# Optimization experiments

Hardware: AMD Instinct MI355X
Metric: run time of the kernel (lower is better)

Reference implementation:

```python
import jax, jax.numpy as jnp
import numpy as np

B, T, C = 2, 2048, 1024
NH = 16

def setup_inputs() -> dict:
    key = jax.random.key(0)
    ks = jax.random.split(key, 5)
    s = 0.02
    return {
        "x": jax.random.normal(ks[0], (B, T, C), dtype=jnp.float32),
        "w_attn": jax.random.normal(ks[1], (C, 3 * C), dtype=jnp.float32) * s,
        "b_attn": jax.random.normal(ks[2], (3 * C,), dtype=jnp.float32) * s,
        "w_proj": jax.random.normal(ks[3], (C, C), dtype=jnp.float32) * s,
        "b_proj": jax.random.normal(ks[4], (C,), dtype=jnp.float32) * s,
        "n_heads": NH,
    }

def reference(x, w_attn, b_attn, w_proj, b_proj, n_heads):
    Bx, Tx, Cx = x.shape
    hd = Cx // n_heads
    qkv = x @ w_attn + b_attn                      # [B,T,3C]
    q, k, v = jnp.split(qkv, 3, axis=-1)
    # [B,T,H,hd] -> [B,H,T,hd]
    q = q.reshape(Bx, Tx, n_heads, hd).transpose(0, 2, 1, 3)
    k = k.reshape(Bx, Tx, n_heads, hd).transpose(0, 2, 1, 3)
    v = v.reshape(Bx, Tx, n_heads, hd).transpose(0, 2, 1, 3)
    scale = 1.0 / np.sqrt(hd).astype(np.float32)
    att = jnp.einsum('bhqd,bhkd->bhqk', q, k) * scale   # [B,H,T,T]
    causal = jnp.tril(jnp.ones((Tx, Tx), dtype=bool))
    att = jnp.where(causal[None, None], att, -jnp.inf)
    att = jax.nn.softmax(att, axis=-1)
    y = jnp.einsum('bhqk,bhkd->bhqd', att, v)            # [B,H,T,hd]
    y = y.transpose(0, 2, 1, 3).reshape(Bx, Tx, Cx)
    return y @ w_proj + b_proj
```

## Files before the change

kernel.cpp:

```cpp
#include <hip/hip_runtime.h>

typedef __bf16 bf16x8 __attribute__((ext_vector_type(8)));
typedef __bf16 bf16x4 __attribute__((ext_vector_type(4)));
typedef float  f32x4  __attribute__((ext_vector_type(4)));
typedef float  f32x16 __attribute__((ext_vector_type(16)));
typedef unsigned int u32;

#define MFMA_BF16(a, b, c) __builtin_amdgcn_mfma_f32_16x16x32_bf16((a), (b), (c), 0, 0, 0)
#define MFMA32(a, b, c) __builtin_amdgcn_mfma_f32_32x32x16_bf16((a), (b), (c), 0, 0, 0)
#define NEG_INF (-1e30f)
#define SCL 0.18033688f

__device__ __forceinline__ void gld16(const void* g, void* l) {
  __builtin_amdgcn_global_load_lds(
      (const __attribute__((address_space(1))) void*)g,
      (__attribute__((address_space(3))) void*)l, 16, 0, 0);
}

__global__ void cast_f32_bf16(const float* __restrict__ in,
                              __bf16* __restrict__ out, int n) {
  int i = (blockIdx.x * 256 + threadIdx.x) * 8;
  if (i >= n) return;
  float4 a = *(const float4*)&in[i];
  float4 b = *(const float4*)&in[i + 4];
  bf16x8 v;
  v[0] = (__bf16)a.x; v[1] = (__bf16)a.y; v[2] = (__bf16)a.z; v[3] = (__bf16)a.w;
  v[4] = (__bf16)b.x; v[5] = (__bf16)b.y; v[6] = (__bf16)b.z; v[7] = (__bf16)b.w;
  *(bf16x8*)&out[i] = v;
}

__global__ void transpose_f32_bf16(const float* __restrict__ in,
                                   __bf16* __restrict__ out, int R, int C) {
  __shared__ float t[32][33];
  int tx = threadIdx.x & 31, ty = threadIdx.x >> 5;
  int x = blockIdx.x * 32 + tx;
  int y0 = blockIdx.y * 32 + ty;
#pragma unroll
  for (int i = 0; i < 4; ++i)
    t[ty + 8 * i][tx] = in[(size_t)(y0 + 8 * i) * C + x];
  __syncthreads();
  int x2 = blockIdx.y * 32 + tx;
#pragma unroll
  for (int i = 0; i < 4; ++i)
    out[(size_t)(blockIdx.x * 32 + ty + 8 * i) * R + x2] = (__bf16)t[tx][ty + 8 * i];
}

#define BN 128
#define BK 64

template <int BMT, typename TC>
__global__ __launch_bounds__(256) void gemm_bt_bias(
    const __bf16* __restrict__ A, const __bf16* __restrict__ Bt,
    const float* __restrict__ bias, TC* __restrict__ Cmat,
    int M, int N, int K) {
  constexpr int NI = BMT / 32;
  __shared__ __align__(16) __bf16 As[BMT * BK];
  __shared__ __align__(16) __bf16 Bs[BN * BK];
  int tid = threadIdx.x;
  int wave = tid >> 6, lane = tid & 63;
  int l16 = lane & 15, quad = lane >> 4;
  int wm = wave >> 1, wn = wave & 1;
  int m0 = blockIdx.y * BMT, n0 = blockIdx.x * BN;

  f32x4 acc[NI][4];
#pragma unroll
  for (int i = 0; i < NI; ++i)
#pragma unroll
    for (int j = 0; j < 4; ++j) acc[i][j] = (f32x4){0.f, 0.f, 0.f, 0.f};

  int row = tid >> 3;
  int kc = ((tid & 7) ^ ((tid >> 3) & 7)) * 8;
  int xr = (l16 & 7) * 8;

  for (int k0 = 0; k0 < K; k0 += BK) {
#pragma unroll
    for (int i = 0; i < NI; ++i)
      gld16(&A[(size_t)(m0 + row + i * 32) * K + k0 + kc],
            (char*)As + (i * 256 + wave * 64) * 16);
#pragma unroll
    for (int j = 0; j < 4; ++j)
      gld16(&Bt[(size_t)(n0 + row + j * 32) * K + k0 + kc],
            (char*)Bs + (j * 256 + wave * 64) * 16);
    __syncthreads();
#pragma unroll
    for (int ks = 0; ks < 2; ++ks) {
      bf16x8 af[NI], bfr[4];
#pragma unroll
      for (int i = 0; i < NI; ++i)
        af[i] = *(const bf16x8*)&As[(wm * (BMT / 2) + i * 16 + l16) * BK +
                                    ((ks * 32 + quad * 8) ^ xr)];
#pragma unroll
      for (int j = 0; j < 4; ++j)
        bfr[j] = *(const bf16x8*)&Bs[(wn * 64 + j * 16 + l16) * BK +
                                     ((ks * 32 + quad * 8) ^ xr)];
#pragma unroll
      for (int i = 0; i < NI; ++i)
#pragma unroll
        for (int j = 0; j < 4; ++j) acc[i][j] = MFMA_BF16(af[i], bfr[j], acc[i][j]);
    }
    __syncthreads();
  }
#pragma unroll
  for (int i = 0; i < NI; ++i) {
#pragma unroll
    for (int j = 0; j < 4; ++j) {
      int col = n0 + wn * 64 + j * 16 + l16;
      float bv = bias[col];
#pragma unroll
      for (int r = 0; r < 4; ++r) {
        int rw = m0 + wm * (BMT / 2) + i * 16 + quad * 4 + r;
        Cmat[(size_t)rw * N + col] = (TC)(acc[i][j][r] + bv);
      }
    }
  }
}

#define BARX do { asm volatile("" ::: "memory"); __builtin_amdgcn_s_barrier(); \
                  asm volatile("" ::: "memory"); } while (0)
#define WLGKM do { asm volatile("s_waitcnt lgkmcnt(0)" ::: "memory"); \
                   __builtin_amdgcn_sched_barrier(0); } while (0)
#define WVM4 asm volatile("s_waitcnt vmcnt(4)" ::: "memory")
#define STA8(SBUF, SKS, T) do { \
    gld16(srcA1 + (size_t)(T) * 64 + (SKS) * 32, (char*)&As[SBUF][SKS][0] + tid * 16); \
    gld16(srcA2 + (size_t)(T) * 64 + (SKS) * 32, (char*)&As[SBUF][SKS][0] + tid * 16 + 8192); \
  } while (0)
#define STB8(SBUF, SKS, T) do { \
    gld16(srcB1 + (size_t)(T) * 64 + (SKS) * 32, (char*)&Bs[SBUF][SKS][0] + tid * 16); \
    gld16(srcB2 + (size_t)(T) * 64 + (SKS) * 32, (char*)&Bs[SBUF][SKS][0] + tid * 16 + 8192); \
  } while (0)
#define LDA4(CBUF, CKS, MQ) do { \
    const __bf16* p_ = &As[CBUF][CKS][(wm * 128 + (MQ) * 64 + l16) * 32 + xrd]; \
    af[0] = *(const bf16x8*)(p_);        af[1] = *(const bf16x8*)(p_ + 512); \
    af[2] = *(const bf16x8*)(p_ + 1024); af[3] = *(const bf16x8*)(p_ + 1536); \
  } while (0)
#define LDB3(CBUF, CKS) do { \
    const __bf16* p_ = &Bs[CBUF][CKS][(wn * 48 + l16) * 32 + xrd]; \
    bfr[0] = *(const bf16x8*)(p_);       bfr[1] = *(const bf16x8*)(p_ + 512); \
    bfr[2] = *(const bf16x8*)(p_ + 1024); \
  } while (0)
#define MM12(MQ) do { \
    __builtin_amdgcn_s_setprio(1); \
    _Pragma("unroll") for (int mi_ = 0; mi_ < 4; ++mi_) \
    _Pragma("unroll") for (int nj_ = 0; nj_ < 3; ++nj_) \
      acc[(MQ) * 4 + mi_][nj_] = MFMA_BF16(af[mi_], bfr[nj_], acc[(MQ) * 4 + mi_][nj_]); \
    __builtin_amdgcn_s_setprio(0); \
  } while (0)

__global__ __launch_bounds__(512, 2) void gemm_qkv_8ph(
    const __bf16* __restrict__ A, const __bf16* __restrict__ Bt,
    const float* __restrict__ bias, __bf16* __restrict__ qkv,
    __bf16* __restrict__ vt) {
  constexpr int GK = 1024, GN = 3072, NT = 16;
  __shared__ __align__(16) __bf16 As[2][2][256 * 32];
  __shared__ __align__(16) __bf16 Bs[2][2][256 * 32];
  const int tid = threadIdx.x;
  const int wave = tid >> 6, lane = tid & 63;
  const int l16 = lane & 15, quad = lane >> 4;
  const int wm = wave >> 2, wn = wave & 3;
  const int m0 = blockIdx.y * 256, n0 = blockIdx.x * 192;

  const int row0 = tid >> 2;
  const int kc = (((tid & 3) ^ ((row0 >> 1) & 3)) * 8);
  const int xrd = (quad ^ ((l16 >> 1) & 3)) * 8;

  const __bf16* srcA1 = A + (size_t)(m0 + row0) * GK + kc;
  const __bf16* srcA2 = srcA1 + (size_t)128 * GK;
  const __bf16* srcB1 = Bt + (size_t)(n0 + row0) * GK + kc;
  const int br2 = (row0 + 128 < 192) ? row0 + 128 : 191;
  const __bf16* srcB2 = Bt + (size_t)(n0 + br2) * GK + kc;

  f32x4 acc[8][3];
#pragma unroll
  for (int m = 0; m < 8; ++m)
#pragma unroll
    for (int n = 0; n < 3; ++n) acc[m][n] = (f32x4){0.f, 0.f, 0.f, 0.f};

  STA8(0, 0, 0); STB8(0, 0, 0);
  STA8(0, 1, 0); STB8(0, 1, 0);
  STA8(1, 0, 1); STB8(1, 0, 1);
  WVM4;
  BARX;

  bf16x8 af[4], bfr[3];
#pragma unroll 1
  for (int i = 0; i < NT / 2; ++i) {
    const int v = 2 * i + 1;
    const int t2 = (2 * i + 2 < NT) ? 2 * i + 2 : NT - 1;
    const int t3 = (2 * i + 3 < NT) ? 2 * i + 3 : NT - 1;
    LDA4(0, 0, 0); LDB3(0, 0); STA8(1, 1, v);
    BARX; WLGKM; MM12(0); BARX;
    LDA4(0, 0, 1); STB8(1, 1, v);
    BARX; WLGKM; MM12(1); BARX;
    LDA4(0, 1, 0); LDB3(0, 1); STA8(0, 0, t2);
    BARX; WLGKM; MM12(0); BARX;
    LDA4(0, 1, 1); STB8(0, 0, t2);
    BARX; WLGKM; MM12(1); WVM4; BARX;
    LDA4(1, 0, 0); LDB3(1, 0); STA8(0, 1, t2);
    BARX; WLGKM; MM12(0); BARX;
    LDA4(1, 0, 1); STB8(0, 1, t2);
    BARX; WLGKM; MM12(1); BARX;
    LDA4(1, 1, 0); LDB3(1, 1); STA8(1, 0, t3);
    BARX; WLGKM; MM12(0); BARX;
    LDA4(1, 1, 1); STB8(1, 0, t3);
    BARX; WLGKM; MM12(1); WVM4; BARX;
  }

#pragma unroll
  for (int n = 0; n < 3; ++n) {
    const int c0 = n0 + wn * 48 + n * 16;
    const int col = c0 + l16;
    const float bv = bias[col];
    if (c0 < 2048) {
#pragma unroll
      for (int m = 0; m < 8; ++m) {
        const int rw = m0 + wm * 128 + m * 16 + quad * 4;
#pragma unroll
        for (int r = 0; r < 4; ++r)
          qkv[(size_t)(rw + r) * GN + col] = (__bf16)(acc[m][n][r] + bv);
      }
    } else {
      const int h = (col - 2048) >> 6, d = col & 63;
#pragma unroll
      for (int m = 0; m < 8; ++m) {
        const int t0 = m0 + wm * 128 + m * 16 + quad * 4;
        const int b = t0 >> 11, tt = t0 & 2047;
        bf16x4 pb;
#pragma unroll
        for (int r = 0; r < 4; ++r) pb[r] = (__bf16)(acc[m][n][r] + bv);
        *(bf16x4*)&vt[(size_t)((b * 16 + h) * 64 + d) * 2048 + tt] = pb;
      }
    }
  }
}

#define CVTPK(D, LO, HI) \
  asm("v_cvt_pk_bf16_f32 %0, %1, %2" : "=v"(D) : "v"(LO), "v"(HI))
#define SWAP32(DST, SRC) \
  asm("v_permlane32_swap_b32 %0, %1" : "+v"(DST), "+v"(SRC))

__device__ __forceinline__ bf16x8 mk8(u32 a, u32 b, u32 c, u32 d) {
  union { u32 u[4]; bf16x8 h; } x;
  x.u[0] = a; x.u[1] = b; x.u[2] = c; x.u[3] = d;
  return x.h;
}

__global__ __launch_bounds__(256, 2) void attn_causal(
    const __bf16* __restrict__ qkv, const __bf16* __restrict__ vt,
    __bf16* __restrict__ y) {
  __shared__ __align__(16) __bf16 Kb[2][2][64 * 64];
  __shared__ __align__(16) __bf16 Vb[2][2][64 * 64];
  const int tid = threadIdx.x;
  const int wave = tid >> 6, lane = tid & 63;
  const int l32 = lane & 31, hi = lane >> 5;
  const int qh = wave >> 1, kh = wave & 1;
  const int bh = blockIdx.x;
  const int b = bh >> 4, h = bh & 15;
  const int RS = 3072;
  const int p = (int)blockIdx.y;

  const int row8 = tid >> 3;
  const int kcs = (((tid & 7) ^ (row8 & 7) ^ ((row8 >> 3) & 3)) * 8);
  const __bf16* kbase = qkv + (size_t)(b * 2048) * RS + 1024 + h * 64 + kcs;
  const __bf16* vbase = vt + (size_t)(bh * 64) * 2048 + kcs;
  const int xr = (l32 & 7) ^ ((l32 >> 3) & 3);
  float* sc = (float*)Vb;

#pragma unroll 1
  for (int phase = 0; phase < 2; ++phase) {
    const int qt = phase ? 31 - p : p;
    const int nit = (qt + 2) >> 1;

    const __bf16* qp = qkv +
        (size_t)(b * 2048 + qt * 64 + qh * 32 + l32) * RS + h * 64 + hi * 8;
    bf16x8 qf[4];
#pragma unroll
    for (int kc = 0; kc < 4; ++kc) qf[kc] = *(const bf16x8*)(qp + kc * 16);

    float l4[4] = {0.f, 0.f, 0.f, 0.f};
    f32x16 o0, o1;
#pragma unroll
    for (int r = 0; r < 16; ++r) { o0[r] = 0.f; o1[r] = 0.f; }

#pragma unroll
    for (int s = 0; s < 2; ++s)
#pragma unroll
      for (int i = 0; i < 2; ++i) {
        gld16(kbase + (size_t)(s * 64 + i * 32 + row8) * RS,
              (char*)Kb[0][s] + (i * 256 + tid) * 16);
        gld16(vbase + (size_t)(i * 32 + row8) * 2048 + s * 64,
              (char*)Vb[0][s] + (i * 256 + tid) * 16);
      }
    __syncthreads();

    for (int it = 0; it < nit; ++it) {
      const int cur = it & 1;
      if (it + 1 < nit) {
        const int kb2 = (it + 1) * 128;
#pragma unroll
        for (int s = 0; s < 2; ++s)
#pragma unroll
          for (int i = 0; i < 2; ++i) {
            gld16(kbase + (size_t)(kb2 + s * 64 + i * 32 + row8) * RS,
                  (char*)Kb[cur ^ 1][s] + (i * 256 + tid) * 16);
            gld16(vbase + (size_t)(i * 32 + row8) * 2048 + kb2 + s * 64,
                  (char*)Vb[cur ^ 1][s] + (i * 256 + tid) * 16);
          }
      }

      const int ktile = 2 * it + kh;
      if (ktile <= qt) {
        f32x16 c0, c1;
#pragma unroll
        for (int r = 0; r < 16; ++r) { c0[r] = 0.f; c1[r] = 0.f; }
        __builtin_amdgcn_s_setprio(1);
#pragma unroll
        for (int kc = 0; kc < 4; ++kc) {
          const int sw = ((kc * 2 + hi) ^ xr) << 3;
          bf16x8 kf0 = *(const bf16x8*)&Kb[cur][kh][l32 * 64 + sw];
          bf16x8 kf1 = *(const bf16x8*)&Kb[cur][kh][(32 + l32) * 64 + sw];
          c0 = MFMA32(kf0, qf[kc], c0);
          c1 = MFMA32(kf1, qf[kc], c1);
        }
        __builtin_amdgcn_s_setprio(0);

        if (ktile == qt) {
          const int qloc = qh * 32 + l32;
#pragma unroll
          for (int r = 0; r < 16; ++r) {
            const int kl = (r & 3) + 8 * (r >> 2) + 4 * hi;
            if (kl > qloc) c0[r] = NEG_INF;
            if (32 + kl > qloc) c1[r] = NEG_INF;
          }
        }

        bf16x8 pb[4];
#pragma unroll
        for (int kb = 0; kb < 2; ++kb) {
          float pv[16];
#pragma unroll
          for (int r = 0; r < 16; ++r) {
            const float sv = (kb ? c1[r] : c0[r]);
            pv[r] = __builtin_amdgcn_exp2f(sv * SCL);
            l4[r & 3] += pv[r];
          }
          u32 a0, a1, b0, b1;
          CVTPK(a0, pv[0], pv[1]);   CVTPK(a1, pv[2], pv[3]);
          CVTPK(b0, pv[4], pv[5]);   CVTPK(b1, pv[6], pv[7]);
          SWAP32(a0, b0); SWAP32(a1, b1);
          pb[kb * 2 + 0] = mk8(a0, a1, b0, b1);
          CVTPK(a0, pv[8], pv[9]);   CVTPK(a1, pv[10], pv[11]);
          CVTPK(b0, pv[12], pv[13]); CVTPK(b1, pv[14], pv[15]);
          SWAP32(a0, b0); SWAP32(a1, b1);
          pb[kb * 2 + 1] = mk8(a0, a1, b0, b1);
        }

        __builtin_amdgcn_s_setprio(1);
#pragma unroll
        for (int kc = 0; kc < 4; ++kc) {
          const int sw = ((kc * 2 + hi) ^ xr) << 3;
          bf16x8 vf0 = *(const bf16x8*)&Vb[cur][kh][l32 * 64 + sw];
          bf16x8 vf1 = *(const bf16x8*)&Vb[cur][kh][(32 + l32) * 64 + sw];
          o0 = MFMA32(vf0, pb[kc], o0);
          o1 = MFMA32(vf1, pb[kc], o1);
        }
        __builtin_amdgcn_s_setprio(0);
      }
      __syncthreads();
    }

    float lred = (l4[0] + l4[1]) + (l4[2] + l4[3]);
    lred += __shfl_xor(lred, 32);
    if (kh == 1) {
      float* ob = sc + qh * 2048;
#pragma unroll
      for (int r = 0; r < 16; ++r) {
        ob[r * 64 + lane] = o0[r];
        ob[1024 + r * 64 + lane] = o1[r];
      }
      if (lane < 32) sc[4096 + qh * 32 + lane] = lred;
    }
    __syncthreads();
    if (kh == 0) {
      const float* ob = sc + qh * 2048;
      lred += sc[4096 + qh * 32 + l32];
      const float inv = 1.f / lred;
      const int orow = b * 2048 + qt * 64 + qh * 32 + l32;
      __bf16* yb = y + (size_t)orow * 1024 + h * 64 + hi * 4;
#pragma unroll
      for (int db = 0; db < 2; ++db) {
#pragma unroll
        for (int g = 0; g < 4; ++g) {
          bf16x4 w;
#pragma unroll
          for (int j = 0; j < 4; ++j) {
            const float v = (db ? o1[g * 4 + j] : o0[g * 4 + j]) +
                            ob[db * 1024 + (g * 4 + j) * 64 + lane];
            w[j] = (__bf16)(v * inv);
          }
          *(bf16x4*)&yb[db * 32 + g * 8] = w;
        }
      }
    }
    __syncthreads();
  }
}

extern "C" void kernel_launch(void* const* d_in, const int* in_sizes, int n_in,
                              void* d_out, int out_size, void* d_ws, size_t ws_size,
                              hipStream_t stream) {
  (void)in_sizes; (void)n_in; (void)out_size; (void)ws_size;
  const float* x      = (const float*)d_in[0];
  const float* w_attn = (const float*)d_in[1];
  const float* b_attn = (const float*)d_in[2];
  const float* w_proj = (const float*)d_in[3];
  const float* b_proj = (const float*)d_in[4];
  float* out = (float*)d_out;

  __bf16* wt_attn = (__bf16*)d_ws;
  __bf16* wt_proj = wt_attn + (size_t)3072 * 1024;
  __bf16* qkv     = wt_proj + (size_t)1024 * 1024;
  __bf16* ybuf    = qkv + (size_t)4096 * 3072;
  __bf16* vtbuf   = ybuf + (size_t)4096 * 1024;

  cast_f32_bf16<<<4096 * 1024 / 2048, 256, 0, stream>>>(x, ybuf, 4096 * 1024);

  transpose_f32_bf16<<<dim3(3072 / 32, 1024 / 32), 256, 0, stream>>>(w_attn, wt_attn, 1024, 3072);
  transpose_f32_bf16<<<dim3(1024 / 32, 1024 / 32), 256, 0, stream>>>(w_proj, wt_proj, 1024, 1024);

  gemm_qkv_8ph<<<dim3(3072 / 192, 4096 / 256), 512, 0, stream>>>(
      ybuf, wt_attn, b_attn, qkv, vtbuf);

  attn_causal<<<dim3(32, 16), 256, 0, stream>>>(qkv, vtbuf, ybuf);

  gemm_bt_bias<64, float><<<dim3(1024 / BN, 4096 / 64), 256, 0, stream>>>(
      ybuf, wt_proj, b_proj, out, 4096, 1024, 1024);
}
```

Baseline: 174.8 us.

## Restructure causal attention into 512-thread blocks over 128-row query tiles

The attention kernel now runs 8 waves per block, each block handling one 128-row query tile, so four query sub-tiles share every K/V tile staged in shared memory. This replaces the old 256-thread scheme in which each block walked two 64-row query tiles (p and 31-p) in sequence. Blocks are ordered with the heaviest causal rows scheduled first to offset the uneven work per block, and the P·V MFMAs are interleaved with each half of the softmax conversion. The aim is better K/V reuse and less per-phase sync and reload overhead. The risks are load imbalance across blocks, register pressure or spills under launch_bounds(512,4), and shared-memory size capping how many blocks fit per CU.

```diff
diff --git a/kernel.cpp b/kernel.cpp
--- a/kernel.cpp
+++ b/kernel.cpp
@@ -244,11 +244,10 @@
   return x.h;
 }
 
-__global__ __launch_bounds__(256, 2) void attn_causal(
+__global__ __launch_bounds__(512, 4) void attn_causal(
     const __bf16* __restrict__ qkv, const __bf16* __restrict__ vt,
     __bf16* __restrict__ y) {
-  __shared__ __align__(16) __bf16 Kb[2][2][64 * 64];
-  __shared__ __align__(16) __bf16 Vb[2][2][64 * 64];
+  __shared__ __align__(16) __bf16 smem[2][2][2][64 * 64];
   const int tid = threadIdx.x;
   const int wave = tid >> 6, lane = tid & 63;
   const int l32 = lane & 31, hi = lane >> 5;
@@ -256,152 +255,147 @@
   const int bh = blockIdx.x;
   const int b = bh >> 4, h = bh & 15;
   const int RS = 3072;
-  const int p = (int)blockIdx.y;
+  const int by = (int)blockIdx.y;
+  const int qb = (by < 8) ? 15 - by : by - 8;
+  const int nit = qb + 1;
+  const int ktmax = 2 * qb + (qh >> 1);
 
   const int row8 = tid >> 3;
   const int kcs = (((tid & 7) ^ (row8 & 7) ^ ((row8 >> 3) & 3)) * 8);
   const __bf16* kbase = qkv + (size_t)(b * 2048) * RS + 1024 + h * 64 + kcs;
   const __bf16* vbase = vt + (size_t)(bh * 64) * 2048 + kcs;
   const int xr = (l32 & 7) ^ ((l32 >> 3) & 3);
-  float* sc = (float*)Vb;
-
-#pragma unroll 1
-  for (int phase = 0; phase < 2; ++phase) {
-    const int qt = phase ? 31 - p : p;
-    const int nit = (qt + 2) >> 1;
-
-    const __bf16* qp = qkv +
-        (size_t)(b * 2048 + qt * 64 + qh * 32 + l32) * RS + h * 64 + hi * 8;
-    bf16x8 qf[4];
-#pragma unroll
-    for (int kc = 0; kc < 4; ++kc) qf[kc] = *(const bf16x8*)(qp + kc * 16);
-
-    float l4[4] = {0.f, 0.f, 0.f, 0.f};
-    f32x16 o0, o1;
-#pragma unroll
-    for (int r = 0; r < 16; ++r) { o0[r] = 0.f; o1[r] = 0.f; }
-
-#pragma unroll
-    for (int s = 0; s < 2; ++s)
-#pragma unroll
-      for (int i = 0; i < 2; ++i) {
-        gld16(kbase + (size_t)(s * 64 + i * 32 + row8) * RS,
-              (char*)Kb[0][s] + (i * 256 + tid) * 16);
-        gld16(vbase + (size_t)(i * 32 + row8) * 2048 + s * 64,
-              (char*)Vb[0][s] + (i * 256 + tid) * 16);
-      }
-    __syncthreads();
-
-    for (int it = 0; it < nit; ++it) {
-      const int cur = it & 1;
-      if (it + 1 < nit) {
-        const int kb2 = (it + 1) * 128;
-#pragma unroll
-        for (int s = 0; s < 2; ++s)
-#pragma unroll
-          for (int i = 0; i < 2; ++i) {
-            gld16(kbase + (size_t)(kb2 + s * 64 + i * 32 + row8) * RS,
-                  (char*)Kb[cur ^ 1][s] + (i * 256 + tid) * 16);
-            gld16(vbase + (size_t)(i * 32 + row8) * 2048 + kb2 + s * 64,
-                  (char*)Vb[cur ^ 1][s] + (i * 256 + tid) * 16);
-          }
-      }
-
-      const int ktile = 2 * it + kh;
-      if (ktile <= qt) {
-        f32x16 c0, c1;
-#pragma unroll
-        for (int r = 0; r < 16; ++r) { c0[r] = 0.f; c1[r] = 0.f; }
+
+  const __bf16* qp = qkv +
+      (size_t)(b * 2048 + qb * 128 + qh * 32 + l32) * RS + h * 64 + hi * 8;
+  bf16x8 qf[4];
+#pragma unroll
+  for (int kc = 0; kc < 4; ++kc) qf[kc] = *(const bf16x8*)(qp + kc * 16);
+
+  float l4[4] = {0.f, 0.f, 0.f, 0.f};
+  f32x16 o0, o1;
+#pragma unroll
+  for (int r = 0; r < 16; ++r) { o0[r] = 0.f; o1[r] = 0.f; }
+
+#pragma unroll
+  for (int s = 0; s < 2; ++s) {
+    gld16(kbase + (size_t)(s * 64 + row8) * RS, (char*)smem[0][0][s] + tid * 16);
+    gld16(vbase + (size_t)row8 * 2048 + s * 64, (char*)smem[1][0][s] + tid * 16);
+  }
+  __syncthreads();
+
+  for (int it = 0; it < nit; ++it) {
+    const int cur = it & 1;
+    if (it < qb) {
+      const int kb2 = (it + 1) * 128;
+#pragma unroll
+      for (int s = 0; s < 2; ++s) {
+        gld16(kbase + (size_t)(kb2 + s * 64 + row8) * RS,
+              (char*)smem[0][cur ^ 1][s] + tid * 16);
+        gld16(vbase + (size_t)row8 * 2048 + kb2 + s * 64,
+              (char*)smem[1][cur ^ 1][s] + tid * 16);
+      }
+    }
+
+    const int kt = 2 * it + kh;
+    if (kt <= ktmax) {
+      const __bf16* Kc = smem[0][cur][kh];
+      const __bf16* Vc = smem[1][cur][kh];
+
+      f32x16 c0, c1;
+#pragma unroll
+      for (int r = 0; r < 16; ++r) { c0[r] = 0.f; c1[r] = 0.f; }
+      __builtin_amdgcn_s_setprio(1);
+#pragma unroll
+      for (int kc = 0; kc < 4; ++kc) {
+        const int sw = ((kc * 2 + hi) ^ xr) << 3;
+        bf16x8 kf0 = *(const bf16x8*)&Kc[l32 * 64 + sw];
+        bf16x8 kf1 = *(const bf16x8*)&Kc[(32 + l32) * 64 + sw];
+        c0 = MFMA32(kf0, qf[kc], c0);
+        c1 = MFMA32(kf1, qf[kc], c1);
+      }
+      __builtin_amdgcn_s_setprio(0);
+
+      if (kt == ktmax) {
+        const int qloc = qh * 32 + l32 - (kt - 2 * qb) * 64;
+#pragma unroll
+        for (int r = 0; r < 16; ++r) {
+          const int kl = (r & 3) + 8 * (r >> 2) + 4 * hi;
+          if (kl > qloc) c0[r] = NEG_INF;
+          if (32 + kl > qloc) c1[r] = NEG_INF;
+        }
+      }
+
+      bf16x8 pb[4];
+#pragma unroll
+      for (int kb = 0; kb < 2; ++kb) {
+        float pv[16];
+#pragma unroll
+        for (int r = 0; r < 16; ++r) {
+          const float sv = (kb ? c1[r] : c0[r]);
+          pv[r] = __builtin_amdgcn_exp2f(sv * SCL);
+          l4[r & 3] += pv[r];
+        }
+        u32 a0, a1, b0, b1;
+        CVTPK(a0, pv[0], pv[1]);   CVTPK(a1, pv[2], pv[3]);
+        CVTPK(b0, pv[4], pv[5]);   CVTPK(b1, pv[6], pv[7]);
+        SWAP32(a0, b0); SWAP32(a1, b1);
+        pb[kb * 2 + 0] = mk8(a0, a1, b0, b1);
+        CVTPK(a0, pv[8], pv[9]);   CVTPK(a1, pv[10], pv[11]);
+        CVTPK(b0, pv[12], pv[13]); CVTPK(b1, pv[14], pv[15]);
+        SWAP32(a0, b0); SWAP32(a1, b1);
+        pb[kb * 2 + 1] = mk8(a0, a1, b0, b1);
+
         __builtin_amdgcn_s_setprio(1);
 #pragma unroll
-        for (int kc = 0; kc < 4; ++kc) {
+        for (int kq = 0; kq < 2; ++kq) {
+          const int kc = kb * 2 + kq;
           const int sw = ((kc * 2 + hi) ^ xr) << 3;
-          bf16x8 kf0 = *(const bf16x8*)&Kb[cur][kh][l32 * 64 + sw];
-          bf16x8 kf1 = *(const bf16x8*)&Kb[cur][kh][(32 + l32) * 64 + sw];
-          c0 = MFMA32(kf0, qf[kc], c0);
-          c1 = MFMA32(kf1, qf[kc], c1);
-        }
-        __builtin_amdgcn_s_setprio(0);
-
-        if (ktile == qt) {
-          const int qloc = qh * 32 + l32;
-#pragma unroll
-          for (int r = 0; r < 16; ++r) {
-            const int kl = (r & 3) + 8 * (r >> 2) + 4 * hi;
-            if (kl > qloc) c0[r] = NEG_INF;
-            if (32 + kl > qloc) c1[r] = NEG_INF;
-          }
-        }
-
-        bf16x8 pb[4];
-#pragma unroll
-        for (int kb = 0; kb < 2; ++kb) {
-          float pv[16];
-#pragma unroll
-          for (int r = 0; r < 16; ++r) {
-            const float sv = (kb ? c1[r] : c0[r]);
-            pv[r] = __builtin_amdgcn_exp2f(sv * SCL);
-            l4[r & 3] += pv[r];
-          }
-          u32 a0, a1, b0, b1;
-          CVTPK(a0, pv[0], pv[1]);   CVTPK(a1, pv[2], pv[3]);
-          CVTPK(b0, pv[4], pv[5]);   CVTPK(b1, pv[6], pv[7]);
-          SWAP32(a0, b0); SWAP32(a1, b1);
-          pb[kb * 2 + 0] = mk8(a0, a1, b0, b1);
-          CVTPK(a0, pv[8], pv[9]);   CVTPK(a1, pv[10], pv[11]);
-          CVTPK(b0, pv[12], pv[13]); CVTPK(b1, pv[14], pv[15]);
-          SWAP32(a0, b0); SWAP32(a1, b1);
-          pb[kb * 2 + 1] = mk8(a0, a1, b0, b1);
-        }
-
-        __builtin_amdgcn_s_setprio(1);
-#pragma unroll
-        for (int kc = 0; kc < 4; ++kc) {
-          const int sw = ((kc * 2 + hi) ^ xr) << 3;
-          bf16x8 vf0 = *(const bf16x8*)&Vb[cur][kh][l32 * 64 + sw];
-          bf16x8 vf1 = *(const bf16x8*)&Vb[cur][kh][(32 + l32) * 64 + sw];
+          bf16x8 vf0 = *(const bf16x8*)&Vc[l32 * 64 + sw];
+          bf16x8 vf1 = *(const bf16x8*)&Vc[(32 + l32) * 64 + sw];
           o0 = MFMA32(vf0, pb[kc], o0);
           o1 = MFMA32(vf1, pb[kc], o1);
         }
         __builtin_amdgcn_s_setprio(0);
       }
-      __syncthreads();
-    }
-
-    float lred = (l4[0] + l4[1]) + (l4[2] + l4[3]);
-    lred += __shfl_xor(lred, 32);
-    if (kh == 1) {
-      float* ob = sc + qh * 2048;
-#pragma unroll
-      for (int r = 0; r < 16; ++r) {
-        ob[r * 64 + lane] = o0[r];
-        ob[1024 + r * 64 + lane] = o1[r];
-      }
-      if (lane < 32) sc[4096 + qh * 32 + lane] = lred;
     }
     __syncthreads();
-    if (kh == 0) {
-      const float* ob = sc + qh * 2048;
-      lred += sc[4096 + qh * 32 + l32];
-      const float inv = 1.f / lred;
-      const int orow = b * 2048 + qt * 64 + qh * 32 + l32;
-      __bf16* yb = y + (size_t)orow * 1024 + h * 64 + hi * 4;
-#pragma unroll
-      for (int db = 0; db < 2; ++db) {
-#pragma unroll
-        for (int g = 0; g < 4; ++g) {
-          bf16x4 w;
-#pragma unroll
-          for (int j = 0; j < 4; ++j) {
-            const float v = (db ? o1[g * 4 + j] : o0[g * 4 + j]) +
-                            ob[db * 1024 + (g * 4 + j) * 64 + lane];
-            w[j] = (__bf16)(v * inv);
-          }
-          *(bf16x4*)&yb[db * 32 + g * 8] = w;
+  }
+
+  float lred = (l4[0] + l4[1]) + (l4[2] + l4[3]);
+  lred += __shfl_xor(lred, 32);
+
+  float* sc = (float*)smem;
+  if (kh == 1) {
+    float* ob = sc + qh * 2048;
+#pragma unroll
+    for (int r = 0; r < 16; ++r) {
+      ob[r * 64 + lane] = o0[r];
+      ob[1024 + r * 64 + lane] = o1[r];
+    }
+    if (lane < 32) sc[8192 + qh * 32 + lane] = lred;
+  }
+  __syncthreads();
+  if (kh == 0) {
+    const float* ob = sc + qh * 2048;
+    lred += sc[8192 + qh * 32 + l32];
+    const float inv = 1.f / lred;
+    const int orow = b * 2048 + qb * 128 + qh * 32 + l32;
+    __bf16* yb = y + (size_t)orow * 1024 + h * 64 + hi * 4;
+#pragma unroll
+    for (int db = 0; db < 2; ++db) {
+#pragma unroll
+      for (int g = 0; g < 4; ++g) {
+        bf16x4 w;
+#pragma unroll
+        for (int j = 0; j < 4; ++j) {
+          const float v = (db ? o1[g * 4 + j] : o0[g * 4 + j]) +
+                          ob[db * 1024 + (g * 4 + j) * 64 + lane];
+          w[j] = (__bf16)(v * inv);
         }
-      }
-    }
-    __syncthreads();
+        *(bf16x4*)&yb[db * 32 + g * 8] = w;
+      }
+    }
   }
 }
 
@@ -430,7 +424,7 @@
   gemm_qkv_8ph<<<dim3(3072 / 192, 4096 / 256), 512, 0, stream>>>(
       ybuf, wt_attn, b_attn, qkv, vtbuf);
 
-  attn_causal<<<dim3(32, 16), 256, 0, stream>>>(qkv, vtbuf, ybuf);
+  attn_causal<<<dim3(32, 16), 512, 0, stream>>>(qkv, vtbuf, ybuf);
 
   gemm_bt_bias<64, float><<<dim3(1024 / BN, 4096 / 64), 256, 0, stream>>>(
       ybuf, wt_proj, b_proj, out, 4096, 1024, 1024);
```

Result: faster. 169.2 us (-3.2%).
